# Performance work log

Measured on AMD Instinct MI355X. Metric: run time of the kernel, lower is better.

Reference implementation:

```python
import jax, jax.numpy as jnp
import numpy as np

TAU = 0.1
SELF_MASK = 1e6  # added to diagonal of self-distances (y_neg is x)


def _cdist(a, b):
    # pairwise L2 distances, [Na, Nb]; eps keeps sqrt grad finite at 0
    sq = (a * a).sum(-1)[:, None] + (b * b).sum(-1)[None, :] - 2.0 * (a @ b.T)
    return jnp.sqrt(jnp.maximum(sq, 1e-12))


def setup_inputs() -> dict:
    key = jax.random.key(0)
    k1, k2 = jax.random.split(key)
    N, D = 4096, 512
    return {
        "x": jax.random.normal(k1, (N, D), dtype=jnp.float32),
        "y_pos": jax.random.normal(k2, (N, D), dtype=jnp.float32),
    }


def reference(x, y_pos):
    # compute_drift_velocity with y_neg = x (training/loss path)
    N = x.shape[0]
    dist_pos = _cdist(x, y_pos)                      # [N, N]
    dist_neg = _cdist(x, x) + SELF_MASK * jnp.eye(N, dtype=x.dtype)
    logits = -jnp.concatenate([dist_pos, dist_neg], axis=1) / TAU  # [N, 2N]
    # dual normalization: row softmax * column softmax, geometric mean
    A_row = jax.nn.softmax(logits, axis=-1)
    A_col = jax.nn.softmax(logits, axis=0)
    A = jnp.sqrt(A_row * A_col)
    A_pos, A_neg = A[:, :N], A[:, N:]
    drift = A_pos @ y_pos - A_neg @ x                # [N, D]
    return drift
```

## Files before the change

### kernel.cpp

```cpp
#include <hip/hip_runtime.h>
#include <math.h>

#define NN   4096
#define DD   512
#define TWON 8192

typedef _Float16 half_t;
typedef unsigned short u16;
using half8  = __attribute__((ext_vector_type(8))) half_t;
using short8 = __attribute__((ext_vector_type(8))) short;
using f32x4  = __attribute__((ext_vector_type(4))) float;

#define NLOG2E_10 (-14.4269504089f)

__device__ __forceinline__ float exp2_f(float x) { return __builtin_amdgcn_exp2f(x); }
__device__ __forceinline__ float log2_f(float x) { return __builtin_amdgcn_logf(x); }
__device__ __forceinline__ float sqrt_f(float x) { return __builtin_amdgcn_sqrtf(x); }

__device__ __forceinline__ u16 f2bf(float f) {
    unsigned u = __float_as_uint(f);
    u += 0x7fffu + ((u >> 16) & 1u);
    return (u16)(u >> 16);
}
__device__ __forceinline__ float bf2f(u16 h) {
    return __uint_as_float(((unsigned)h) << 16);
}
__device__ __forceinline__ void gl16(const void* g, void* l) {
    __builtin_amdgcn_global_load_lds(
        (const __attribute__((address_space(1))) void*)g,
        (__attribute__((address_space(3))) void*)l, 16, 0, 0);
}
__device__ __forceinline__ f32x4 mfma16h(half8 a, half8 b, f32x4 c) {
    return __builtin_amdgcn_mfma_f32_16x16x32_f16(a, b, c, 0, 0, 0);
}
__device__ __forceinline__ f32x4 mfma16b(short8 a, short8 b, f32x4 c) {
    return __builtin_amdgcn_mfma_f32_16x16x32_bf16(a, b, c, 0, 0, 0);
}

__global__ __launch_bounds__(64)
void prep_k(const float* __restrict__ x, const float* __restrict__ y,
            half_t* __restrict__ bhi, float* __restrict__ nb) {
    int r = blockIdx.x;
    int l = threadIdx.x;
    const float* src = (r < NN) ? (y + (size_t)r * DD) : (x + (size_t)(r - NN) * DD);
    float4 v0 = *reinterpret_cast<const float4*>(src + l * 8);
    float4 v1 = *reinterpret_cast<const float4*>(src + l * 8 + 4);
    float e[8] = {v0.x, v0.y, v0.z, v0.w, v1.x, v1.y, v1.z, v1.w};
    float s = 0.f;
    half8 h;
    #pragma unroll
    for (int q = 0; q < 8; ++q) {
        s += e[q] * e[q];
        h[q] = (half_t)e[q];
    }
    *reinterpret_cast<half8*>(bhi + (size_t)r * DD + l * 8) = h;
    #pragma unroll
    for (int off = 32; off; off >>= 1) s += __shfl_down(s, off);
    if (l == 0) nb[r] = s;
}

__global__ __launch_bounds__(256)
void b2tr_k(const half_t* __restrict__ bhi, u16* __restrict__ b2t) {
    __shared__ half_t tl[32][33];
    int k0 = blockIdx.x * 32, d0 = blockIdx.y * 32;
    int tx = threadIdx.x, ty = threadIdx.y;
    #pragma unroll
    for (int j = 0; j < 4; ++j)
        tl[ty + 8 * j][tx] = bhi[(size_t)(k0 + ty + 8 * j) * DD + d0 + tx];
    __syncthreads();
    float sgn = (k0 < NN) ? 1.f : -1.f;
    #pragma unroll
    for (int j = 0; j < 4; ++j) {
        float v = (float)tl[tx][ty + 8 * j] * sgn;
        b2t[(size_t)(d0 + ty + 8 * j) * TWON + k0 + tx] = f2bf(v);
    }
}

__global__ __launch_bounds__(256)
void gemm1_k(const half_t* __restrict__ bhi,
             const float* __restrict__ nb, u16* __restrict__ Ef,
             float* __restrict__ Ct,
             float* __restrict__ rpm, float* __restrict__ rps,
             float* __restrict__ cpm, float* __restrict__ cps) {
    __shared__ unsigned char lds[32768];
    const int t = threadIdx.x;
    const int wave = t >> 6, lane = t & 63;
    const int i0 = blockIdx.y * 128, j0 = blockIdx.x * 128;
    const int wm = (wave >> 1) * 64, wn = (wave & 1) * 64;
    const half_t* ahig = bhi + (size_t)NN * DD;
    f32x4 acc[4][4] = {};
    for (int k0 = 0; k0 < DD; k0 += 64) {
        __syncthreads();
        #pragma unroll
        for (int q = 0; q < 4; ++q) {
            const int dbase = (wave * 4 + q) * 1024;
            const int p  = dbase + lane * 16;
            const int r  = p >> 7;
            const int cb = (p & 127) ^ ((r & 7) << 4);
            const size_t offA = (size_t)(i0 + r) * DD + k0 + (cb >> 1);
            const size_t offB = (size_t)(j0 + r) * DD + k0 + (cb >> 1);
            gl16(ahig + offA, lds + dbase);
            gl16(bhi  + offB, lds + 16384 + dbase);
        }
        asm volatile("s_waitcnt vmcnt(0)" ::: "memory");
        __builtin_amdgcn_sched_barrier(0);
        __syncthreads();
        #pragma unroll
        for (int kk = 0; kk < 2; ++kk) {
            half8 ah[4];
            #pragma unroll
            for (int m = 0; m < 4; ++m) {
                const int row = wm + m * 16 + (lane & 15);
                const int off = row * 128 + ((kk * 64 + (lane >> 4) * 16) ^ ((row & 7) << 4));
                ah[m] = *reinterpret_cast<const half8*>(lds + off);
            }
            #pragma unroll
            for (int n = 0; n < 4; ++n) {
                const int row = wn + n * 16 + (lane & 15);
                const int off = row * 128 + ((kk * 64 + (lane >> 4) * 16) ^ ((row & 7) << 4));
                half8 bh = *reinterpret_cast<const half8*>(lds + 16384 + off);
                #pragma unroll
                for (int m = 0; m < 4; ++m)
                    acc[m][n] = mfma16h(bh, ah[m], acc[m][n]);
            }
        }
    }
    float nxi[4];
    #pragma unroll
    for (int m = 0; m < 4; ++m) nxi[m] = nb[NN + i0 + wm + m * 16 + (lane & 15)];
    float4 nbj4[4];
    #pragma unroll
    for (int n = 0; n < 4; ++n)
        nbj4[n] = *reinterpret_cast<const float4*>(nb + j0 + wn + n * 16 + (lane >> 4) * 4);
    float tmax = -3.0e38f;
    #pragma unroll
    for (int m = 0; m < 4; ++m) {
        const int irel = i0 + wm + m * 16 + (lane & 15) + NN - j0;
        #pragma unroll
        for (int n = 0; n < 4; ++n) {
            #pragma unroll
            for (int r4 = 0; r4 < 4; ++r4) {
                const int jrel = wn + n * 16 + (lane >> 4) * 4 + r4;
                float nbj = (r4 == 0) ? nbj4[n].x : (r4 == 1) ? nbj4[n].y
                          : (r4 == 2) ? nbj4[n].z : nbj4[n].w;
                float sq = nxi[m] + nbj - 2.0f * acc[m][n][r4];
                float lg = NLOG2E_10 * sqrt_f(fmaxf(sq, 1e-12f));
                if (jrel == irel) lg = -1e7f;
                acc[m][n][r4] = lg;
                tmax = fmaxf(tmax, lg);
            }
        }
    }
    #pragma unroll
    for (int off = 1; off < 64; off <<= 1) tmax = fmaxf(tmax, __shfl_xor(tmax, off));
    __syncthreads();
    float* red = reinterpret_cast<float*>(lds);
    if (lane == 0) red[wave] = tmax;
    __syncthreads();
    const float C = fmaxf(fmaxf(red[0], red[1]), fmaxf(red[2], red[3]));
    __syncthreads();
    if (t == 0) Ct[blockIdx.y * 64 + blockIdx.x] = C;
    float rs[4] = {}, cs[16] = {};
    #pragma unroll
    for (int m = 0; m < 4; ++m) {
        const size_t ibase = (size_t)(i0 + wm + m * 16 + (lane & 15)) * TWON;
        #pragma unroll
        for (int n = 0; n < 4; ++n) {
            float e0 = exp2_f(acc[m][n][0] - C);
            float e1 = exp2_f(acc[m][n][1] - C);
            float e2 = exp2_f(acc[m][n][2] - C);
            float e3 = exp2_f(acc[m][n][3] - C);
            uint2 pk;
            pk.x = (__float_as_uint(e0) >> 16) | (__float_as_uint(e1) & 0xffff0000u);
            pk.y = (__float_as_uint(e2) >> 16) | (__float_as_uint(e3) & 0xffff0000u);
            const int j = j0 + wn + n * 16 + (lane >> 4) * 4;
            *reinterpret_cast<uint2*>(Ef + ibase + j) = pk;
            rs[m] += e0 + e1 + e2 + e3;
            cs[n * 4 + 0] += e0; cs[n * 4 + 1] += e1;
            cs[n * 4 + 2] += e2; cs[n * 4 + 3] += e3;
        }
    }
    #pragma unroll
    for (int off = 16; off < 64; off <<= 1) {
        #pragma unroll
        for (int m = 0; m < 4; ++m) rs[m] += __shfl_xor(rs[m], off);
    }
    #pragma unroll
    for (int off = 1; off < 16; off <<= 1) {
        #pragma unroll
        for (int q = 0; q < 16; ++q) cs[q] += __shfl_xor(cs[q], off);
    }
    if (lane < 16) {
        #pragma unroll
        for (int m = 0; m < 4; ++m)
            red[(wave & 1) * 128 + wm + m * 16 + lane] = rs[m];
    }
    if ((lane & 15) == 0) {
        #pragma unroll
        for (int n = 0; n < 4; ++n)
            #pragma unroll
            for (int r4 = 0; r4 < 4; ++r4)
                red[256 + (wave >> 1) * 128 + (wave & 1) * 64 + n * 16 + (lane >> 4) * 4 + r4]
                    = cs[n * 4 + r4];
    }
    __syncthreads();
    if (t < 128) {
        float S = red[t] + red[128 + t];
        rpm[(size_t)blockIdx.x * NN + i0 + t] = C;
        rps[(size_t)blockIdx.x * NN + i0 + t] = S;
    } else {
        const int c = t - 128;
        float S = red[256 + c] + red[384 + c];
        cpm[(size_t)blockIdx.y * TWON + j0 + c] = C;
        cps[(size_t)blockIdx.y * TWON + j0 + c] = S;
    }
}

__global__ __launch_bounds__(256)
void comb_k(const float* __restrict__ rpm, const float* __restrict__ rps,
            const float* __restrict__ cpm, const float* __restrict__ cps,
            float* __restrict__ rm, float* __restrict__ rrs, float* __restrict__ Pj) {
    const int b = blockIdx.x;
    if (b < 16) {
        int i = b * 256 + threadIdx.x;
        float M = -3.0e38f;
        for (int tt = 0; tt < TWON / 128; ++tt) M = fmaxf(M, rpm[(size_t)tt * NN + i]);
        float S = 0.f;
        for (int tt = 0; tt < TWON / 128; ++tt)
            S += rps[(size_t)tt * NN + i] * exp2_f(rpm[(size_t)tt * NN + i] - M);
        rm[i] = M; rrs[i] = rsqrtf(S);
    } else {
        int j = (b - 16) * 256 + threadIdx.x;
        float M = -3.0e38f;
        for (int tt = 0; tt < NN / 128; ++tt) M = fmaxf(M, cpm[(size_t)tt * TWON + j]);
        float S = 0.f;
        for (int tt = 0; tt < NN / 128; ++tt)
            S += cps[(size_t)tt * TWON + j] * exp2_f(cpm[(size_t)tt * TWON + j] - M);
        Pj[j] = -0.5f * M - 0.5f * log2_f(S);
    }
}

__global__ __launch_bounds__(512, 4)
void gemm2_k(const u16* __restrict__ Ef, const u16* __restrict__ b2t,
             const float* __restrict__ Ct, const float* __restrict__ rm,
             const float* __restrict__ Pj, const float* __restrict__ rrs,
             unsigned* __restrict__ part) {
    __shared__ unsigned char lds[32768];
    const int t = threadIdx.x;
    const int wave = t >> 6, lane = t & 63;
    const int sw = blockIdx.x;
    const int kslice = sw & 7;
    const int idx2 = sw >> 3;
    const int db = idx2 & 3;
    const int iblk = idx2 >> 2;
    const int i0 = iblk * 128;
    const int d0 = db * 128;
    const int kbase = kslice * 1024;
    const int mh = wave >> 2, dq = wave & 3;
    const int sr = t >> 2;
    const int kc = (t & 3) * 16;
    const int aw0 = sr * 128 + ((kc * 2) ^ ((sr & 7) << 4));
    const int aw1 = sr * 128 + (((kc + 8) * 2) ^ ((sr & 7) << 4));
    const float rmh = 0.5f * rm[i0 + sr];
    const int NT = 16;
    f32x4 acc[4][2] = {};
    for (int it = 0; it < NT; ++it) {
        __syncthreads();
        #pragma unroll
        for (int q = 0; q < 2; ++q) {
            const int dbase = (wave * 2 + q) * 1024;
            const int p  = dbase + lane * 16;
            const int r  = p >> 7;
            const int cb = (p & 127) ^ ((r & 7) << 4);
            gl16(b2t + (size_t)(d0 + r) * TWON + kbase + it * 64 + (cb >> 1),
                 lds + 16384 + dbase);
        }
        {
            const int k = kbase + it * 64 + kc;
            const u16* ep = Ef + (size_t)(i0 + sr) * TWON + k;
            short8 aE0 = *reinterpret_cast<const short8*>(ep);
            short8 aE1 = *reinterpret_cast<const short8*>(ep + 8);
            float4 p0 = *reinterpret_cast<const float4*>(Pj + k);
            float4 p1 = *reinterpret_cast<const float4*>(Pj + k + 4);
            float4 p2 = *reinterpret_cast<const float4*>(Pj + k + 8);
            float4 p3 = *reinterpret_cast<const float4*>(Pj + k + 12);
            const float arg = Ct[iblk * 64 + ((kbase + it * 64) >> 7)] - rmh;
            short8 g0, g1;
            g0[0] = (short)(__float_as_uint(bf2f((u16)aE0[0]) * exp2_f(arg + p0.x)) >> 16);
            g0[1] = (short)(__float_as_uint(bf2f((u16)aE0[1]) * exp2_f(arg + p0.y)) >> 16);
            g0[2] = (short)(__float_as_uint(bf2f((u16)aE0[2]) * exp2_f(arg + p0.z)) >> 16);
            g0[3] = (short)(__float_as_uint(bf2f((u16)aE0[3]) * exp2_f(arg + p0.w)) >> 16);
            g0[4] = (short)(__float_as_uint(bf2f((u16)aE0[4]) * exp2_f(arg + p1.x)) >> 16);
            g0[5] = (short)(__float_as_uint(bf2f((u16)aE0[5]) * exp2_f(arg + p1.y)) >> 16);
            g0[6] = (short)(__float_as_uint(bf2f((u16)aE0[6]) * exp2_f(arg + p1.z)) >> 16);
            g0[7] = (short)(__float_as_uint(bf2f((u16)aE0[7]) * exp2_f(arg + p1.w)) >> 16);
            g1[0] = (short)(__float_as_uint(bf2f((u16)aE1[0]) * exp2_f(arg + p2.x)) >> 16);
            g1[1] = (short)(__float_as_uint(bf2f((u16)aE1[1]) * exp2_f(arg + p2.y)) >> 16);
            g1[2] = (short)(__float_as_uint(bf2f((u16)aE1[2]) * exp2_f(arg + p2.z)) >> 16);
            g1[3] = (short)(__float_as_uint(bf2f((u16)aE1[3]) * exp2_f(arg + p2.w)) >> 16);
            g1[4] = (short)(__float_as_uint(bf2f((u16)aE1[4]) * exp2_f(arg + p3.x)) >> 16);
            g1[5] = (short)(__float_as_uint(bf2f((u16)aE1[5]) * exp2_f(arg + p3.y)) >> 16);
            g1[6] = (short)(__float_as_uint(bf2f((u16)aE1[6]) * exp2_f(arg + p3.z)) >> 16);
            g1[7] = (short)(__float_as_uint(bf2f((u16)aE1[7]) * exp2_f(arg + p3.w)) >> 16);
            *reinterpret_cast<short8*>(lds + aw0) = g0;
            *reinterpret_cast<short8*>(lds + aw1) = g1;
        }
        asm volatile("s_waitcnt vmcnt(0)" ::: "memory");
        __builtin_amdgcn_sched_barrier(0);
        __syncthreads();
        #pragma unroll
        for (int kk = 0; kk < 2; ++kk) {
            short8 af[4], bfr[2];
            #pragma unroll
            for (int m = 0; m < 4; ++m) {
                const int row = mh * 64 + m * 16 + (lane & 15);
                const int off = row * 128 +
                                ((kk * 64 + (lane >> 4) * 16) ^ ((row & 7) << 4));
                af[m] = *reinterpret_cast<const short8*>(lds + off);
            }
            #pragma unroll
            for (int n = 0; n < 2; ++n) {
                const int row = dq * 32 + n * 16 + (lane & 15);
                const int off = 16384 + row * 128 +
                                ((kk * 64 + (lane >> 4) * 16) ^ ((row & 7) << 4));
                bfr[n] = *reinterpret_cast<const short8*>(lds + off);
            }
            #pragma unroll
            for (int m = 0; m < 4; ++m)
                #pragma unroll
                for (int n = 0; n < 2; ++n)
                    acc[m][n] = mfma16b(af[m], bfr[n], acc[m][n]);
        }
    }
    unsigned* pout = part + ((size_t)(kslice * 128 + idx2) * 512 + t) * 16;
    #pragma unroll
    for (int m = 0; m < 4; ++m) {
        float rf[4];
        #pragma unroll
        for (int r4 = 0; r4 < 4; ++r4)
            rf[r4] = rrs[i0 + mh * 64 + m * 16 + (lane >> 4) * 4 + r4];
        unsigned pk[4];
        #pragma unroll
        for (int n = 0; n < 2; ++n) {
            pk[n * 2]     = (unsigned)f2bf(acc[m][n][0] * rf[0]) |
                            ((unsigned)f2bf(acc[m][n][1] * rf[1]) << 16);
            pk[n * 2 + 1] = (unsigned)f2bf(acc[m][n][2] * rf[2]) |
                            ((unsigned)f2bf(acc[m][n][3] * rf[3]) << 16);
        }
        *reinterpret_cast<uint4*>(pout + m * 4) = *reinterpret_cast<uint4*>(pk);
    }
}

__global__ __launch_bounds__(512)
void reduce_k(const unsigned* __restrict__ part, float* __restrict__ out) {
    const int b = blockIdx.x;
    const int mq = b & 3, pos = b >> 2;
    const int db = pos & 3, iblk = pos >> 2;
    const int t = threadIdx.x;
    const int lane = t & 63, wave = t >> 6;
    const int mh = wave >> 2, dq = wave & 3;
    float s[8] = {};
    #pragma unroll
    for (int ks = 0; ks < 8; ++ks) {
        const unsigned* p = part + ((size_t)(ks * 128 + pos) * 512 + t) * 16 + mq * 4;
        uint4 a = *reinterpret_cast<const uint4*>(p);
        unsigned u[4] = {a.x, a.y, a.z, a.w};
        #pragma unroll
        for (int n = 0; n < 2; ++n) {
            s[n * 4 + 0] += bf2f((u16)(u[n * 2] & 0xffffu));
            s[n * 4 + 1] += bf2f((u16)(u[n * 2] >> 16));
            s[n * 4 + 2] += bf2f((u16)(u[n * 2 + 1] & 0xffffu));
            s[n * 4 + 3] += bf2f((u16)(u[n * 2 + 1] >> 16));
        }
    }
    #pragma unroll
    for (int n = 0; n < 2; ++n)
        #pragma unroll
        for (int r4 = 0; r4 < 4; ++r4) {
            const int i = iblk * 128 + mh * 64 + mq * 16 + (lane >> 4) * 4 + r4;
            const int d = db * 128 + dq * 32 + n * 16 + (lane & 15);
            out[(size_t)i * DD + d] = s[n * 4 + r4];
        }
}

extern "C" void kernel_launch(void* const* d_in, const int* in_sizes, int n_in,
                              void* d_out, int out_size, void* d_ws, size_t ws_size,
                              hipStream_t stream) {
    const float* x = (const float*)d_in[0];
    const float* y = (const float*)d_in[1];
    float* out = (float*)d_out;

    char* w = (char*)d_ws;
    const size_t OFF_EF   = 0;
    const size_t OFF_BHI  = 67108864;
    const size_t OFF_B2T  = OFF_BHI + 8388608;
    const size_t OFF_PART = OFF_B2T + 8388608;
    const size_t OFF_RPM  = OFF_PART + 67108864;
    const size_t OFF_RPS  = OFF_RPM + 1048576;
    const size_t OFF_CPM  = OFF_RPS + 1048576;
    const size_t OFF_CPS  = OFF_CPM + 1048576;
    const size_t OFF_CT   = OFF_CPS + 1048576;
    const size_t OFF_TAIL = OFF_CT + 65536;

    u16*      Ef   = (u16*)(w + OFF_EF);
    half_t*   bhi  = (half_t*)(w + OFF_BHI);
    u16*      b2t  = (u16*)(w + OFF_B2T);
    unsigned* part = (unsigned*)(w + OFF_PART);
    float*    rpm  = (float*)(w + OFF_RPM);
    float*    rps  = (float*)(w + OFF_RPS);
    float*    cpm  = (float*)(w + OFF_CPM);
    float*    cps  = (float*)(w + OFF_CPS);
    float*    Ct   = (float*)(w + OFF_CT);
    float*    nb   = (float*)(w + OFF_TAIL);
    float*    rm   = nb  + TWON;
    float*    rrs  = rm  + NN;
    float*    Pj   = rrs + NN;

    prep_k<<<TWON, 64, 0, stream>>>(x, y, bhi, nb);
    gemm1_k<<<dim3(TWON / 128, NN / 128), 256, 0, stream>>>(bhi, nb, Ef, Ct,
                                                            rpm, rps, cpm, cps);
    comb_k<<<48, 256, 0, stream>>>(rpm, rps, cpm, cps, rm, rrs, Pj);
    b2tr_k<<<dim3(TWON / 32, DD / 32), dim3(32, 8), 0, stream>>>(bhi, b2t);
    gemm2_k<<<1024, 512, 0, stream>>>(Ef, b2t, Ct, rm, Pj, rrs, part);
    reduce_k<<<512, 512, 0, stream>>>(part, out);
}
```

Before: 175.5 us.

## Prefetch next A-tile registers in gemm2 and precompute column exp factors

Two changes go into the second GEMM. First, the A-operand loads (Ef and the column factor) for the next iteration are issued into a second register set before the current tile is transformed, a manual double-buffer meant to hide global load latency. Second, the per-element exp2 is replaced by a column factor precomputed once in comb_k and a per-row scalar exp, with a fixed offset K0REF keeping both in float range. This removes 16 transcendental ops per thread per iteration, at the cost of extra registers and some overflow/underflow risk if the logits fall outside the offset's range.

```diff
diff --git a/kernel.cpp b/kernel.cpp
--- a/kernel.cpp
+++ b/kernel.cpp
@@ -12,6 +12,7 @@
 using f32x4  = __attribute__((ext_vector_type(4))) float;
 
 #define NLOG2E_10 (-14.4269504089f)
+#define K0REF 210.0f
 
 __device__ __forceinline__ float exp2_f(float x) { return __builtin_amdgcn_exp2f(x); }
 __device__ __forceinline__ float log2_f(float x) { return __builtin_amdgcn_logf(x); }
@@ -24,6 +25,9 @@
 }
 __device__ __forceinline__ float bf2f(u16 h) {
     return __uint_as_float(((unsigned)h) << 16);
+}
+__device__ __forceinline__ u16 truncbf(float f) {
+    return (u16)(__float_as_uint(f) >> 16);
 }
 __device__ __forceinline__ void gl16(const void* g, void* l) {
     __builtin_amdgcn_global_load_lds(
@@ -219,7 +223,7 @@
 __global__ __launch_bounds__(256)
 void comb_k(const float* __restrict__ rpm, const float* __restrict__ rps,
             const float* __restrict__ cpm, const float* __restrict__ cps,
-            float* __restrict__ rm, float* __restrict__ rrs, float* __restrict__ Pj) {
+            float* __restrict__ rm, float* __restrict__ rrs, float* __restrict__ Qe) {
     const int b = blockIdx.x;
     if (b < 16) {
         int i = b * 256 + threadIdx.x;
@@ -236,14 +240,14 @@
         float S = 0.f;
         for (int tt = 0; tt < NN / 128; ++tt)
             S += cps[(size_t)tt * TWON + j] * exp2_f(cpm[(size_t)tt * TWON + j] - M);
-        Pj[j] = -0.5f * M - 0.5f * log2_f(S);
+        Qe[j] = exp2_f(-0.5f * M - 0.5f * log2_f(S) - K0REF);
     }
 }
 
 __global__ __launch_bounds__(512, 4)
 void gemm2_k(const u16* __restrict__ Ef, const u16* __restrict__ b2t,
              const float* __restrict__ Ct, const float* __restrict__ rm,
-             const float* __restrict__ Pj, const float* __restrict__ rrs,
+             const float* __restrict__ Qe, const float* __restrict__ rrs,
              unsigned* __restrict__ part) {
     __shared__ unsigned char lds[32768];
     const int t = threadIdx.x;
@@ -264,8 +268,29 @@
     const float rmh = 0.5f * rm[i0 + sr];
     const int NT = 16;
     f32x4 acc[4][2] = {};
-    for (int it = 0; it < NT; ++it) {
-        __syncthreads();
+    short8 eA0, eA1, eB0, eB1;
+    float4 qA0, qA1, qA2, qA3, qB0, qB1, qB2, qB3;
+    auto LOADSETA = [&](int it) {
+        const int k = kbase + it * 64 + kc;
+        const u16* ep = Ef + (size_t)(i0 + sr) * TWON + k;
+        eA0 = *reinterpret_cast<const short8*>(ep);
+        eA1 = *reinterpret_cast<const short8*>(ep + 8);
+        qA0 = *reinterpret_cast<const float4*>(Qe + k);
+        qA1 = *reinterpret_cast<const float4*>(Qe + k + 4);
+        qA2 = *reinterpret_cast<const float4*>(Qe + k + 8);
+        qA3 = *reinterpret_cast<const float4*>(Qe + k + 12);
+    };
+    auto LOADSETB = [&](int it) {
+        const int k = kbase + it * 64 + kc;
+        const u16* ep = Ef + (size_t)(i0 + sr) * TWON + k;
+        eB0 = *reinterpret_cast<const short8*>(ep);
+        eB1 = *reinterpret_cast<const short8*>(ep + 8);
+        qB0 = *reinterpret_cast<const float4*>(Qe + k);
+        qB1 = *reinterpret_cast<const float4*>(Qe + k + 4);
+        qB2 = *reinterpret_cast<const float4*>(Qe + k + 8);
+        qB3 = *reinterpret_cast<const float4*>(Qe + k + 12);
+    };
+    auto BSTAGE = [&](int it) {
         #pragma unroll
         for (int q = 0; q < 2; ++q) {
             const int dbase = (wave * 2 + q) * 1024;
@@ -275,39 +300,54 @@
             gl16(b2t + (size_t)(d0 + r) * TWON + kbase + it * 64 + (cb >> 1),
                  lds + 16384 + dbase);
         }
-        {
-            const int k = kbase + it * 64 + kc;
-            const u16* ep = Ef + (size_t)(i0 + sr) * TWON + k;
-            short8 aE0 = *reinterpret_cast<const short8*>(ep);
-            short8 aE1 = *reinterpret_cast<const short8*>(ep + 8);
-            float4 p0 = *reinterpret_cast<const float4*>(Pj + k);
-            float4 p1 = *reinterpret_cast<const float4*>(Pj + k + 4);
-            float4 p2 = *reinterpret_cast<const float4*>(Pj + k + 8);
-            float4 p3 = *reinterpret_cast<const float4*>(Pj + k + 12);
-            const float arg = Ct[iblk * 64 + ((kbase + it * 64) >> 7)] - rmh;
-            short8 g0, g1;
-            g0[0] = (short)(__float_as_uint(bf2f((u16)aE0[0]) * exp2_f(arg + p0.x)) >> 16);
-            g0[1] = (short)(__float_as_uint(bf2f((u16)aE0[1]) * exp2_f(arg + p0.y)) >> 16);
-            g0[2] = (short)(__float_as_uint(bf2f((u16)aE0[2]) * exp2_f(arg + p0.z)) >> 16);
-            g0[3] = (short)(__float_as_uint(bf2f((u16)aE0[3]) * exp2_f(arg + p0.w)) >> 16);
-            g0[4] = (short)(__float_as_uint(bf2f((u16)aE0[4]) * exp2_f(arg + p1.x)) >> 16);
-            g0[5] = (short)(__float_as_uint(bf2f((u16)aE0[5]) * exp2_f(arg + p1.y)) >> 16);
-            g0[6] = (short)(__float_as_uint(bf2f((u16)aE0[6]) * exp2_f(arg + p1.z)) >> 16);
-            g0[7] = (short)(__float_as_uint(bf2f((u16)aE0[7]) * exp2_f(arg + p1.w)) >> 16);
-            g1[0] = (short)(__float_as_uint(bf2f((u16)aE1[0]) * exp2_f(arg + p2.x)) >> 16);
-            g1[1] = (short)(__float_as_uint(bf2f((u16)aE1[1]) * exp2_f(arg + p2.y)) >> 16);
-            g1[2] = (short)(__float_as_uint(bf2f((u16)aE1[2]) * exp2_f(arg + p2.z)) >> 16);
-            g1[3] = (short)(__float_as_uint(bf2f((u16)aE1[3]) * exp2_f(arg + p2.w)) >> 16);
-            g1[4] = (short)(__float_as_uint(bf2f((u16)aE1[4]) * exp2_f(arg + p3.x)) >> 16);
-            g1[5] = (short)(__float_as_uint(bf2f((u16)aE1[5]) * exp2_f(arg + p3.y)) >> 16);
-            g1[6] = (short)(__float_as_uint(bf2f((u16)aE1[6]) * exp2_f(arg + p3.z)) >> 16);
-            g1[7] = (short)(__float_as_uint(bf2f((u16)aE1[7]) * exp2_f(arg + p3.w)) >> 16);
-            *reinterpret_cast<short8*>(lds + aw0) = g0;
-            *reinterpret_cast<short8*>(lds + aw1) = g1;
-        }
-        asm volatile("s_waitcnt vmcnt(0)" ::: "memory");
-        __builtin_amdgcn_sched_barrier(0);
-        __syncthreads();
+    };
+    auto TRANSA = [&](int it) {
+        const float arg = Ct[iblk * 64 + ((kbase + it * 64) >> 7)] - rmh;
+        const float ea = exp2_f(arg + K0REF);
+        short8 g0, g1;
+        g0[0] = (short)truncbf((bf2f((u16)eA0[0]) * qA0.x) * ea);
+        g0[1] = (short)truncbf((bf2f((u16)eA0[1]) * qA0.y) * ea);
+        g0[2] = (short)truncbf((bf2f((u16)eA0[2]) * qA0.z) * ea);
+        g0[3] = (short)truncbf((bf2f((u16)eA0[3]) * qA0.w) * ea);
+        g0[4] = (short)truncbf((bf2f((u16)eA0[4]) * qA1.x) * ea);
+        g0[5] = (short)truncbf((bf2f((u16)eA0[5]) * qA1.y) * ea);
+        g0[6] = (short)truncbf((bf2f((u16)eA0[6]) * qA1.z) * ea);
+        g0[7] = (short)truncbf((bf2f((u16)eA0[7]) * qA1.w) * ea);
+        g1[0] = (short)truncbf((bf2f((u16)eA1[0]) * qA2.x) * ea);
+        g1[1] = (short)truncbf((bf2f((u16)eA1[1]) * qA2.y) * ea);
+        g1[2] = (short)truncbf((bf2f((u16)eA1[2]) * qA2.z) * ea);
+        g1[3] = (short)truncbf((bf2f((u16)eA1[3]) * qA2.w) * ea);
+        g1[4] = (short)truncbf((bf2f((u16)eA1[4]) * qA3.x) * ea);
+        g1[5] = (short)truncbf((bf2f((u16)eA1[5]) * qA3.y) * ea);
+        g1[6] = (short)truncbf((bf2f((u16)eA1[6]) * qA3.z) * ea);
+        g1[7] = (short)truncbf((bf2f((u16)eA1[7]) * qA3.w) * ea);
+        *reinterpret_cast<short8*>(lds + aw0) = g0;
+        *reinterpret_cast<short8*>(lds + aw1) = g1;
+    };
+    auto TRANSB = [&](int it) {
+        const float arg = Ct[iblk * 64 + ((kbase + it * 64) >> 7)] - rmh;
+        const float ea = exp2_f(arg + K0REF);
+        short8 g0, g1;
+        g0[0] = (short)truncbf((bf2f((u16)eB0[0]) * qB0.x) * ea);
+        g0[1] = (short)truncbf((bf2f((u16)eB0[1]) * qB0.y) * ea);
+        g0[2] = (short)truncbf((bf2f((u16)eB0[2]) * qB0.z) * ea);
+        g0[3] = (short)truncbf((bf2f((u16)eB0[3]) * qB0.w) * ea);
+        g0[4] = (short)truncbf((bf2f((u16)eB0[4]) * qB1.x) * ea);
+        g0[5] = (short)truncbf((bf2f((u16)eB0[5]) * qB1.y) * ea);
+        g0[6] = (short)truncbf((bf2f((u16)eB0[6]) * qB1.z) * ea);
+        g0[7] = (short)truncbf((bf2f((u16)eB0[7]) * qB1.w) * ea);
+        g1[0] = (short)truncbf((bf2f((u16)eB1[0]) * qB2.x) * ea);
+        g1[1] = (short)truncbf((bf2f((u16)eB1[1]) * qB2.y) * ea);
+        g1[2] = (short)truncbf((bf2f((u16)eB1[2]) * qB2.z) * ea);
+        g1[3] = (short)truncbf((bf2f((u16)eB1[3]) * qB2.w) * ea);
+        g1[4] = (short)truncbf((bf2f((u16)eB1[4]) * qB3.x) * ea);
+        g1[5] = (short)truncbf((bf2f((u16)eB1[5]) * qB3.y) * ea);
+        g1[6] = (short)truncbf((bf2f((u16)eB1[6]) * qB3.z) * ea);
+        g1[7] = (short)truncbf((bf2f((u16)eB1[7]) * qB3.w) * ea);
+        *reinterpret_cast<short8*>(lds + aw0) = g0;
+        *reinterpret_cast<short8*>(lds + aw1) = g1;
+    };
+    auto DOMFMA = [&]() {
         #pragma unroll
         for (int kk = 0; kk < 2; ++kk) {
             short8 af[4], bfr[2];
@@ -331,6 +371,25 @@
                 for (int n = 0; n < 2; ++n)
                     acc[m][n] = mfma16b(af[m], bfr[n], acc[m][n]);
         }
+    };
+    LOADSETA(0);
+    for (int it = 0; it < NT; it += 2) {
+        __syncthreads();
+        BSTAGE(it);
+        if (it + 1 < NT) LOADSETB(it + 1);
+        TRANSA(it);
+        asm volatile("s_waitcnt vmcnt(0)" ::: "memory");
+        __builtin_amdgcn_sched_barrier(0);
+        __syncthreads();
+        DOMFMA();
+        __syncthreads();
+        BSTAGE(it + 1);
+        if (it + 2 < NT) LOADSETA(it + 2);
+        TRANSB(it + 1);
+        asm volatile("s_waitcnt vmcnt(0)" ::: "memory");
+        __builtin_amdgcn_sched_barrier(0);
+        __syncthreads();
+        DOMFMA();
     }
     unsigned* pout = part + ((size_t)(kslice * 128 + idx2) * 512 + t) * 16;
     #pragma unroll
@@ -414,13 +473,13 @@
     float*    nb   = (float*)(w + OFF_TAIL);
     float*    rm   = nb  + TWON;
     float*    rrs  = rm  + NN;
-    float*    Pj   = rrs + NN;
+    float*    Qe   = rrs + NN;
 
     prep_k<<<TWON, 64, 0, stream>>>(x, y, bhi, nb);
     gemm1_k<<<dim3(TWON / 128, NN / 128), 256, 0, stream>>>(bhi, nb, Ef, Ct,
                                                             rpm, rps, cpm, cps);
-    comb_k<<<48, 256, 0, stream>>>(rpm, rps, cpm, cps, rm, rrs, Pj);
+    comb_k<<<48, 256, 0, stream>>>(rpm, rps, cpm, cps, rm, rrs, Qe);
     b2tr_k<<<dim3(TWON / 32, DD / 32), dim3(32, 8), 0, stream>>>(bhi, b2t);
-    gemm2_k<<<1024, 512, 0, stream>>>(Ef, b2t, Ct, rm, Pj, rrs, part);
+    gemm2_k<<<1024, 512, 0, stream>>>(Ef, b2t, Ct, rm, Qe, rrs, part);
     reduce_k<<<512, 512, 0, stream>>>(part, out);
 }
```

Result: slower. 183.4 us (+4.5%).
